# Optimization experiments

Measured on AMD Instinct MI355X. Metric: run time of the kernel, lower is better.

The kernel has to match this reference:

```python
import jax, jax.numpy as jnp
import numpy as np

NCONST = 100
NFEATS = 16
NCLASS = 5
NEFF = 6
NDYN = 6
BN_EPS = 1e-3  # keras BatchNormalization default epsilon


def _edge_indices(nconst):
    # itertools.product order, skipping self-pairs, matching _build_relation_matrices
    recv, send = [], []
    for i in range(nconst):
        for j in range(nconst):
            if i != j:
                recv.append(i)
                send.append(j)
    return np.asarray(recv, np.int32), np.asarray(send, np.int32)


def setup_inputs() -> dict:
    key = jax.random.key(0)
    ks = jax.random.split(key, 16)

    def w(k, shape, fan_in):
        return (jax.random.normal(k, shape, jnp.float32) / np.sqrt(fan_in)).astype(jnp.float32)

    inp = {
        "x": jax.random.normal(ks[0], (512, NCONST, NFEATS), jnp.float32),
        # batchnorm (inference-mode) params over the feature axis
        "bn_gamma": jnp.ones((NFEATS,), jnp.float32),
        "bn_beta": jnp.zeros((NFEATS,), jnp.float32),
        "bn_mean": jnp.zeros((NFEATS,), jnp.float32),
        "bn_var": jnp.ones((NFEATS,), jnp.float32),
        # fr: pointwise Conv1D == dense over last dim; 2*nfeats -> 30 -> 15 -> 6
        "fr_w1": w(ks[1], (2 * NFEATS, 30), 2 * NFEATS), "fr_b1": jnp.zeros((30,), jnp.float32),
        "fr_w2": w(ks[2], (30, 15), 30), "fr_b2": jnp.zeros((15,), jnp.float32),
        "fr_w3": w(ks[3], (15, NEFF), 15), "fr_b3": jnp.zeros((NEFF,), jnp.float32),
        # fo: (nfeats + neffects) -> 45 -> 22 -> 6
        "fo_w1": w(ks[4], (NFEATS + NEFF, 45), NFEATS + NEFF), "fo_b1": jnp.zeros((45,), jnp.float32),
        "fo_w2": w(ks[5], (45, 22), 45), "fo_b2": jnp.zeros((22,), jnp.float32),
        "fo_w3": w(ks[6], (22, NDYN), 22), "fo_b3": jnp.zeros((NDYN,), jnp.float32),
        # fc: ndyn -> 48 -> nclasses (softmax)
        "fc_w1": w(ks[7], (NDYN, 48), NDYN), "fc_b1": jnp.zeros((48,), jnp.float32),
        "fc_w2": w(ks[8], (48, NCLASS), 48), "fc_b2": jnp.zeros((NCLASS,), jnp.float32),
    }
    return inp


def reference(x, bn_gamma, bn_beta, bn_mean, bn_var,
              fr_w1, fr_b1, fr_w2, fr_b2, fr_w3, fr_b3,
              fo_w1, fo_b1, fo_w2, fo_b2, fo_w3, fo_b3,
              fc_w1, fc_b1, fc_w2, fc_b2):
    nconst = x.shape[1]
    recv_idx, send_idx = _edge_indices(nconst)  # static, shape (nedges,)

    # BatchNormalization (inference) over the feature axis: (B, N, F)
    xb = (x - bn_mean) * jax.lax.rsqrt(bn_var + BN_EPS) * bn_gamma + bn_beta

    # One-hot relation matmuls are exact gathers: (B, E, F) each.
    # Concat order matches Concatenate(axis=1)([receiver, sender]) pre-permute.
    fr_in = jnp.concatenate([xb[:, recv_idx, :], xb[:, send_idx, :]], axis=-1)  # (B, E, 2F)

    h = jax.nn.relu(fr_in @ fr_w1 + fr_b1)
    h = jax.nn.relu(h @ fr_w2 + fr_b2)
    effects = jax.nn.relu(h @ fr_w3 + fr_b3)  # (B, E, neff)

    # Multiplying by receiver_matrix^T is a scatter-add of edge effects to receiver nodes.
    agg = jnp.zeros((x.shape[0], nconst, effects.shape[-1]), effects.dtype)
    agg = agg.at[:, recv_idx, :].add(effects)  # (B, N, neff)

    fo_in = jnp.concatenate([xb, agg], axis=-1)  # (B, N, F + neff)
    d = jax.nn.relu(fo_in @ fo_w1 + fo_b1)
    d = jax.nn.relu(d @ fo_w2 + fo_b2)
    d = jax.nn.relu(d @ fo_w3 + fo_b3)  # (B, N, ndyn)

    fc_in = jnp.sum(d, axis=1)  # summation=True -> (B, ndyn)
    h = jax.nn.relu(fc_in @ fc_w1 + fc_b1)
    logits = h @ fc_w2 + fc_b2
    return jax.nn.softmax(logits, axis=-1)  # (B, nclasses)
```

## Files before the change

kernel.cpp:

```cpp
#include <hip/hip_runtime.h>
#include <math.h>

#define NCONST 100
#define NF     16
#define BLK    512

typedef _Float16 f16;
typedef _Float16 f16x8 __attribute__((ext_vector_type(8)));
typedef _Float16 f16x4 __attribute__((ext_vector_type(4)));
typedef float    f32x16 __attribute__((ext_vector_type(16)));

__global__ __launch_bounds__(BLK, 4) void convint_fused(
    const float* __restrict__ x,
    const float* __restrict__ bn_g, const float* __restrict__ bn_b,
    const float* __restrict__ bn_m, const float* __restrict__ bn_v,
    const float* __restrict__ frw1, const float* __restrict__ frb1,
    const float* __restrict__ frw2, const float* __restrict__ frb2,
    const float* __restrict__ frw3, const float* __restrict__ frb3,
    const float* __restrict__ fow1, const float* __restrict__ fob1,
    const float* __restrict__ fow2, const float* __restrict__ fob2,
    const float* __restrict__ fow3, const float* __restrict__ fob3,
    const float* __restrict__ fcw1, const float* __restrict__ fcb1,
    const float* __restrict__ fcw2, const float* __restrict__ fcb2,
    float* __restrict__ out)
{
    __shared__ float xbn[NCONST][NF];
    __shared__ float upool[7200];
    __shared__ float aggF[NCONST * 8];
    __shared__ float fcin[8];
    __shared__ float hfc[48];
    __shared__ float logits[8];

    char* const PrB = (char*)upool;
    char* const PsB = PrB + 8000;
    float (*const foh1)[48] = (float (*)[48])upool;
    float (*const foh2)[24] = (float (*)[24])(upool + 4800);

    const int b   = blockIdx.x;
    const int tid = threadIdx.x;
    const float* xb = x + (size_t)b * (NCONST * NF);

    for (int idx = tid; idx < NCONST * NF; idx += BLK) {
        int f = idx & 15;
        float sc = rsqrtf(bn_v[f] + 1e-3f) * bn_g[f];
        xbn[idx >> 4][f] = (xb[idx] - bn_m[f]) * sc + bn_b[f];
    }
    if (tid < 8) fcin[tid] = 0.f;
    __syncthreads();

    for (int idx = tid; idx < 1600; idx += BLK) {
        int n   = idx >> 4;
        int rem = idx & 15;
        int sel = rem >> 3;
        int oq  = rem & 7;
        int o0  = oq * 4;

        float xs[16];
        {
            const float4* xv = (const float4*)(&xbn[n][0]);
            float4 x0 = xv[0], x1 = xv[1], x2 = xv[2], x3 = xv[3];
            xs[0]=x0.x; xs[1]=x0.y; xs[2]=x0.z; xs[3]=x0.w;
            xs[4]=x1.x; xs[5]=x1.y; xs[6]=x1.z; xs[7]=x1.w;
            xs[8]=x2.x; xs[9]=x2.y; xs[10]=x2.z; xs[11]=x2.w;
            xs[12]=x3.x; xs[13]=x3.y; xs[14]=x3.z; xs[15]=x3.w;
        }
        float acc0 = (!sel) ? frb1[o0 + 0] : 0.f;
        float acc1 = (!sel) ? frb1[o0 + 1] : 0.f;
        float acc2 = (!sel && oq < 7) ? frb1[o0 + 2] : 0.f;
        float acc3 = (!sel && oq < 7) ? frb1[o0 + 3] : 0.f;
        const float* wbase = frw1 + sel * 16 * 30;
        const int wcol2 = (oq < 7) ? o0 + 2 : 28;
        #pragma unroll
        for (int f = 0; f < 16; ++f) {
            const float* wr = wbase + f * 30;
            float2 wa = *(const float2*)(wr + o0);
            float2 wb = *(const float2*)(wr + wcol2);
            acc0 = fmaf(xs[f], wa.x, acc0);
            acc1 = fmaf(xs[f], wa.y, acc1);
            acc2 = fmaf(xs[f], wb.x, acc2);
            acc3 = fmaf(xs[f], wb.y, acc3);
        }
        f16x4 hv;
        hv[0] = (f16)acc0;
        hv[1] = (f16)acc1;
        hv[2] = (oq < 7) ? (f16)acc2 : (sel ? (f16)0.f : (f16)1.f);
        hv[3] = (oq < 7) ? (f16)acc3 : (f16)0.f;
        int slot = oq >> 1;
        int sw = (slot & 2) | ((slot ^ (n >> 3)) & 1);
        *(f16x4*)((sel ? PsB : PrB) + n * 80 + sw * 16 + (oq & 1) * 8) = hv;
    }
    __syncthreads();

    {
        const int l  = tid & 63;
        const int wv = tid >> 6;
        const int e  = l & 31;
        const int hi = l >> 5;

        const int eC  = (e < 15) ? e : 14;
        const int eC3 = (e < 6)  ? e : 5;

        f16x8 bf1a, bf1b, bf2;
        #pragma unroll
        for (int m = 0; m < 8; ++m) {
            int ka  = hi * 8 + m;
            int kb_ = 16 + ka;
            float wa = frw2[ka * 15 + eC];
            float wb = (kb_ < 30) ? frw2[kb_ * 15 + eC] : frb2[eC];
            float w3 = (ka  < 15) ? frw3[ka * 6 + eC3]  : frb3[eC3];
            bf1a[m] = (e < 15)              ? (f16)wa : (f16)0.f;
            bf1b[m] = (e < 15 && kb_ < 31)  ? (f16)wb : (f16)0.f;
            bf2[m]  = (e < 6)               ? (f16)w3 : (f16)0.f;
        }
        f32x16 cz;
        #pragma unroll
        for (int r = 0; r < 16; ++r) cz[r] = 0.f;

        for (int i = wv; i < NCONST; i += 8) {
            const int pi = (i >> 3) & 1;
            const char* prp = PrB + i * 80 + ((hi ^ pi) * 16);
            f16x8 pra = *(const f16x8*)prp;
            f16x8 prb = *(const f16x8*)(prp + 32);
            float2 r2[2];
            r2[0].x = 0.f; r2[0].y = 0.f; r2[1].x = 0.f; r2[1].y = 0.f;

            int j = i + 1 + e; if (j >= 100) j -= 100;
            #pragma unroll
            for (int tb = 0; tb < 4; ++tb) {
                const int pj = (j >> 3) & 1;
                const char* psp = PsB + j * 80 + ((hi ^ pj) * 16);
                f16x8 psa = *(const f16x8*)psp;
                f16x8 psb = *(const f16x8*)(psp + 32);
                f16x8 h1a = pra + psa;
                f16x8 h1b = prb + psb;
                #pragma unroll
                for (int m = 0; m < 8; ++m) {
                    h1a[m] = (h1a[m] > (f16)0.f) ? h1a[m] : (f16)0.f;
                    h1b[m] = (h1b[m] > (f16)0.f) ? h1b[m] : (f16)0.f;
                }
                f32x16 c1 = __builtin_amdgcn_mfma_f32_32x32x16_f16(bf1a, h1a, cz, 0, 0, 0);
                c1 = __builtin_amdgcn_mfma_f32_32x32x16_f16(bf1b, h1b, c1, 0, 0, 0);

                float v7 = hi ? 1.0f : fmaxf(c1[7], 0.f);
                int pw0 = __builtin_bit_cast(int, __builtin_amdgcn_cvt_pkrtz(fmaxf(c1[0], 0.f), fmaxf(c1[1], 0.f)));
                int pw1 = __builtin_bit_cast(int, __builtin_amdgcn_cvt_pkrtz(fmaxf(c1[2], 0.f), fmaxf(c1[3], 0.f)));
                int pw2 = __builtin_bit_cast(int, __builtin_amdgcn_cvt_pkrtz(fmaxf(c1[4], 0.f), fmaxf(c1[5], 0.f)));
                int pw3 = __builtin_bit_cast(int, __builtin_amdgcn_cvt_pkrtz(fmaxf(c1[6], 0.f), v7));
                int s0 = hi ? pw0 : pw2;
                int s1 = hi ? pw1 : pw3;
                int r0 = __shfl_xor(s0, 32);
                int r1 = __shfl_xor(s1, 32);
                union { int w[4]; f16x8 v; } a2;
                a2.w[0] = hi ? r0  : pw0;
                a2.w[1] = hi ? r1  : pw1;
                a2.w[2] = hi ? pw2 : r0;
                a2.w[3] = hi ? pw3 : r1;

                f32x16 c2 = __builtin_amdgcn_mfma_f32_32x32x16_f16(a2.v, bf2, cz, 0, 0, 0);

                if (tb < 3) {
                    #pragma unroll
                    for (int p = 0; p < 8; ++p) {
                        r2[p & 1].x += fmaxf(c2[2 * p],     0.f);
                        r2[p & 1].y += fmaxf(c2[2 * p + 1], 0.f);
                    }
                } else if (hi == 0) {
                    r2[0].x += fmaxf(c2[0], 0.f);
                    r2[0].y += fmaxf(c2[1], 0.f);
                    r2[1].x += fmaxf(c2[2], 0.f);
                }
                j += 32; if (j >= 100) j -= 100;
            }
            float s = r2[0].x + r2[0].y + r2[1].x + r2[1].y;
            s += __shfl_xor(s, 32);
            if (hi == 0 && e < 6) aggF[i * 8 + e] = s;
        }
    }
    __syncthreads();

    for (int idx = tid; idx < NCONST * 45; idx += BLK) {
        int n = idx / 45, o = idx - n * 45;
        float acc = fob1[o];
        const float4* xv = (const float4*)(&xbn[n][0]);
        #pragma unroll
        for (int q = 0; q < 4; ++q) {
            float4 xq = xv[q];
            acc = fmaf(xq.x, fow1[(4 * q + 0) * 45 + o], acc);
            acc = fmaf(xq.y, fow1[(4 * q + 1) * 45 + o], acc);
            acc = fmaf(xq.z, fow1[(4 * q + 2) * 45 + o], acc);
            acc = fmaf(xq.w, fow1[(4 * q + 3) * 45 + o], acc);
        }
        const float4 a0 = *(const float4*)(&aggF[n * 8]);
        const float2 a1 = *(const float2*)(&aggF[n * 8 + 4]);
        acc = fmaf(a0.x, fow1[16 * 45 + o], acc);
        acc = fmaf(a0.y, fow1[17 * 45 + o], acc);
        acc = fmaf(a0.z, fow1[18 * 45 + o], acc);
        acc = fmaf(a0.w, fow1[19 * 45 + o], acc);
        acc = fmaf(a1.x, fow1[20 * 45 + o], acc);
        acc = fmaf(a1.y, fow1[21 * 45 + o], acc);
        foh1[n][o] = fmaxf(acc, 0.f);
    }
    __syncthreads();

    for (int idx = tid; idx < NCONST * 22; idx += BLK) {
        int n = idx / 22, o = idx - n * 22;
        float acc = fob2[o];
        const float4* hv = (const float4*)(&foh1[n][0]);
        #pragma unroll
        for (int q = 0; q < 11; ++q) {
            float4 h4 = hv[q];
            acc = fmaf(h4.x, fow2[(4 * q + 0) * 22 + o], acc);
            acc = fmaf(h4.y, fow2[(4 * q + 1) * 22 + o], acc);
            acc = fmaf(h4.z, fow2[(4 * q + 2) * 22 + o], acc);
            acc = fmaf(h4.w, fow2[(4 * q + 3) * 22 + o], acc);
        }
        acc = fmaf(foh1[n][44], fow2[44 * 22 + o], acc);
        foh2[n][o] = fmaxf(acc, 0.f);
    }
    __syncthreads();

    for (int idx = tid; idx < NCONST * 6; idx += BLK) {
        int n = idx / 6, c = idx - n * 6;
        float acc = fob3[c];
        const float4* hv = (const float4*)(&foh2[n][0]);
        #pragma unroll
        for (int q = 0; q < 5; ++q) {
            float4 h4 = hv[q];
            acc = fmaf(h4.x, fow3[(4 * q + 0) * 6 + c], acc);
            acc = fmaf(h4.y, fow3[(4 * q + 1) * 6 + c], acc);
            acc = fmaf(h4.z, fow3[(4 * q + 2) * 6 + c], acc);
            acc = fmaf(h4.w, fow3[(4 * q + 3) * 6 + c], acc);
        }
        acc = fmaf(foh2[n][20], fow3[20 * 6 + c], acc);
        acc = fmaf(foh2[n][21], fow3[21 * 6 + c], acc);
        atomicAdd(&fcin[c], fmaxf(acc, 0.f));
    }
    __syncthreads();

    if (tid < 48) {
        float acc = fcb1[tid];
        #pragma unroll
        for (int k = 0; k < 6; ++k) acc = fmaf(fcin[k], fcw1[k * 48 + tid], acc);
        hfc[tid] = fmaxf(acc, 0.f);
    }
    __syncthreads();
    if (tid < 5) {
        float acc = fcb2[tid];
        #pragma unroll
        for (int k = 0; k < 48; ++k) acc = fmaf(hfc[k], fcw2[k * 5 + tid], acc);
        logits[tid] = acc;
    }
    __syncthreads();
    if (tid == 0) {
        float m = logits[0];
        #pragma unroll
        for (int c = 1; c < 5; ++c) m = fmaxf(m, logits[c]);
        float ex[5], sum = 0.f;
        #pragma unroll
        for (int c = 0; c < 5; ++c) { ex[c] = __expf(logits[c] - m); sum += ex[c]; }
        float inv = 1.f / sum;
        #pragma unroll
        for (int c = 0; c < 5; ++c) out[(size_t)b * 5 + c] = ex[c] * inv;
    }
}

extern "C" void kernel_launch(void* const* d_in, const int* in_sizes, int n_in,
                              void* d_out, int out_size, void* d_ws, size_t ws_size,
                              hipStream_t stream) {
    const float* x     = (const float*)d_in[0];
    const float* bn_g  = (const float*)d_in[1];
    const float* bn_b  = (const float*)d_in[2];
    const float* bn_m  = (const float*)d_in[3];
    const float* bn_v  = (const float*)d_in[4];
    const float* frw1  = (const float*)d_in[5];
    const float* frb1  = (const float*)d_in[6];
    const float* frw2  = (const float*)d_in[7];
    const float* frb2  = (const float*)d_in[8];
    const float* frw3  = (const float*)d_in[9];
    const float* frb3  = (const float*)d_in[10];
    const float* fow1  = (const float*)d_in[11];
    const float* fob1  = (const float*)d_in[12];
    const float* fow2  = (const float*)d_in[13];
    const float* fob2  = (const float*)d_in[14];
    const float* fow3  = (const float*)d_in[15];
    const float* fob3  = (const float*)d_in[16];
    const float* fcw1  = (const float*)d_in[17];
    const float* fcb1  = (const float*)d_in[18];
    const float* fcw2  = (const float*)d_in[19];
    const float* fcb2  = (const float*)d_in[20];

    const int B = in_sizes[0] / (NCONST * NF);

    convint_fused<<<dim3(B), dim3(BLK), 0, stream>>>(
        x, bn_g, bn_b, bn_m, bn_v,
        frw1, frb1, frw2, frb2, frw3, frb3,
        fow1, fob1, fow2, fob2, fow3, fob3,
        fcw1, fcb1, fcw2, fcb2,
        (float*)d_out);
}
```

Baseline: 67.92 us.

## Split fused kernel into projection, edge, and output kernels via workspace

The single fused per-sample kernel becomes three kernels. The first computes the receiver/sender first-layer projections across two blocks per sample and writes them to a global workspace in fp16. The second runs the MFMA edge network with 1024-thread blocks (16 waves instead of 8) and writes the aggregated effects to global memory. The third recomputes batchnorm and runs the node and classifier MLPs. The aim is more parallelism and occupancy in each phase, at the cost of extra launches and global round-trips through the workspace.

```diff
diff --git a/kernel.cpp b/kernel.cpp
--- a/kernel.cpp
+++ b/kernel.cpp
@@ -3,20 +3,187 @@
 
 #define NCONST 100
 #define NF     16
-#define BLK    512
 
 typedef _Float16 f16;
 typedef _Float16 f16x8 __attribute__((ext_vector_type(8)));
 typedef _Float16 f16x4 __attribute__((ext_vector_type(4)));
 typedef float    f32x16 __attribute__((ext_vector_type(16)));
 
-__global__ __launch_bounds__(BLK, 4) void convint_fused(
+
+__global__ __launch_bounds__(512, 2) void k1_proj(
     const float* __restrict__ x,
     const float* __restrict__ bn_g, const float* __restrict__ bn_b,
     const float* __restrict__ bn_m, const float* __restrict__ bn_v,
     const float* __restrict__ frw1, const float* __restrict__ frb1,
+    f16* __restrict__ prps)
+{
+    __shared__ float xs[50][16];
+    const int b   = blockIdx.y;
+    const int n0  = blockIdx.x * 50;
+    const int tid = threadIdx.x;
+
+    for (int idx = tid; idx < 50 * 16; idx += 512) {
+        int f = idx & 15;
+        float sc = rsqrtf(bn_v[f] + 1e-3f) * bn_g[f];
+        xs[idx >> 4][f] = (x[((size_t)b * NCONST + n0) * NF + idx] - bn_m[f]) * sc + bn_b[f];
+    }
+    __syncthreads();
+
+    for (int idx = tid; idx < 800; idx += 512) {
+        int nL  = idx >> 4;
+        int rem = idx & 15;
+        int sel = rem >> 3;
+        int oq  = rem & 7;
+        int o0  = oq * 4;
+        int n   = n0 + nL;
+
+        float xv[16];
+        {
+            const float4* xp = (const float4*)(&xs[nL][0]);
+            float4 x0 = xp[0], x1 = xp[1], x2 = xp[2], x3 = xp[3];
+            xv[0]=x0.x; xv[1]=x0.y; xv[2]=x0.z; xv[3]=x0.w;
+            xv[4]=x1.x; xv[5]=x1.y; xv[6]=x1.z; xv[7]=x1.w;
+            xv[8]=x2.x; xv[9]=x2.y; xv[10]=x2.z; xv[11]=x2.w;
+            xv[12]=x3.x; xv[13]=x3.y; xv[14]=x3.z; xv[15]=x3.w;
+        }
+        float acc0 = (!sel) ? frb1[o0 + 0] : 0.f;
+        float acc1 = (!sel) ? frb1[o0 + 1] : 0.f;
+        float acc2 = (!sel && oq < 7) ? frb1[o0 + 2] : 0.f;
+        float acc3 = (!sel && oq < 7) ? frb1[o0 + 3] : 0.f;
+        const float* wbase = frw1 + sel * 16 * 30;
+        const int wcol2 = (oq < 7) ? o0 + 2 : 28;
+        #pragma unroll
+        for (int f = 0; f < 16; ++f) {
+            const float* wr = wbase + f * 30;
+            float2 wa = *(const float2*)(wr + o0);
+            float2 wb = *(const float2*)(wr + wcol2);
+            acc0 = fmaf(xv[f], wa.x, acc0);
+            acc1 = fmaf(xv[f], wa.y, acc1);
+            acc2 = fmaf(xv[f], wb.x, acc2);
+            acc3 = fmaf(xv[f], wb.y, acc3);
+        }
+        f16x4 hv;
+        hv[0] = (f16)acc0;
+        hv[1] = (f16)acc1;
+        hv[2] = (oq < 7) ? (f16)acc2 : (sel ? (f16)0.f : (f16)1.f);
+        hv[3] = (oq < 7) ? (f16)acc3 : (f16)0.f;
+        int slot = oq >> 1;
+        int sw = (slot & 2) | ((slot ^ (n >> 3)) & 1);
+        *(f16x4*)(prps + (size_t)b * 8192 + sel * 4000 + n * 40 + sw * 8 + (oq & 1) * 4) = hv;
+    }
+}
+
+__global__ __launch_bounds__(1024, 2) void k2_edge(
+    const f16* __restrict__ prps,
     const float* __restrict__ frw2, const float* __restrict__ frb2,
     const float* __restrict__ frw3, const float* __restrict__ frb3,
+    float* __restrict__ agg)
+{
+    __shared__ char P[16000];
+
+    const int b   = blockIdx.x;
+    const int tid = threadIdx.x;
+    {
+        const float4* src = (const float4*)(prps + (size_t)b * 8192);
+        float4* dst = (float4*)P;
+        if (tid < 1000) dst[tid] = src[tid];
+    }
+    __syncthreads();
+
+    const char* PrB = (const char*)P;
+    const char* PsB = (const char*)P + 8000;
+
+    const int l  = tid & 63;
+    const int wv = tid >> 6;
+    const int e  = l & 31;
+    const int hi = l >> 5;
+
+    const int eC  = (e < 15) ? e : 14;
+    const int eC3 = (e < 6)  ? e : 5;
+
+    f16x8 bf1a, bf1b, bf2;
+    #pragma unroll
+    for (int m = 0; m < 8; ++m) {
+        int ka  = hi * 8 + m;
+        int kb_ = 16 + ka;
+        float wa = frw2[ka * 15 + eC];
+        float wb = (kb_ < 30) ? frw2[kb_ * 15 + eC] : frb2[eC];
+        float w3 = (ka  < 15) ? frw3[ka * 6 + eC3]  : frb3[eC3];
+        bf1a[m] = (e < 15)              ? (f16)wa : (f16)0.f;
+        bf1b[m] = (e < 15 && kb_ < 31)  ? (f16)wb : (f16)0.f;
+        bf2[m]  = (e < 6)               ? (f16)w3 : (f16)0.f;
+    }
+    f32x16 cz;
+    #pragma unroll
+    for (int r = 0; r < 16; ++r) cz[r] = 0.f;
+
+    for (int i = wv; i < NCONST; i += 16) {
+        const int pi = (i >> 3) & 1;
+        const char* prp = PrB + i * 80 + ((hi ^ pi) * 16);
+        f16x8 pra = *(const f16x8*)prp;
+        f16x8 prb = *(const f16x8*)(prp + 32);
+        float2 r2[2];
+        r2[0].x = 0.f; r2[0].y = 0.f; r2[1].x = 0.f; r2[1].y = 0.f;
+
+        int j = i + 1 + e; if (j >= 100) j -= 100;
+        #pragma unroll
+        for (int tb = 0; tb < 4; ++tb) {
+            const int pj = (j >> 3) & 1;
+            const char* psp = PsB + j * 80 + ((hi ^ pj) * 16);
+            f16x8 psa = *(const f16x8*)psp;
+            f16x8 psb = *(const f16x8*)(psp + 32);
+            f16x8 h1a = pra + psa;
+            f16x8 h1b = prb + psb;
+            #pragma unroll
+            for (int m = 0; m < 8; ++m) {
+                h1a[m] = (h1a[m] > (f16)0.f) ? h1a[m] : (f16)0.f;
+                h1b[m] = (h1b[m] > (f16)0.f) ? h1b[m] : (f16)0.f;
+            }
+            f32x16 c1 = __builtin_amdgcn_mfma_f32_32x32x16_f16(bf1a, h1a, cz, 0, 0, 0);
+            c1 = __builtin_amdgcn_mfma_f32_32x32x16_f16(bf1b, h1b, c1, 0, 0, 0);
+
+            float v7 = hi ? 1.0f : fmaxf(c1[7], 0.f);
+            int pw0 = __builtin_bit_cast(int, __builtin_amdgcn_cvt_pkrtz(fmaxf(c1[0], 0.f), fmaxf(c1[1], 0.f)));
+            int pw1 = __builtin_bit_cast(int, __builtin_amdgcn_cvt_pkrtz(fmaxf(c1[2], 0.f), fmaxf(c1[3], 0.f)));
+            int pw2 = __builtin_bit_cast(int, __builtin_amdgcn_cvt_pkrtz(fmaxf(c1[4], 0.f), fmaxf(c1[5], 0.f)));
+            int pw3 = __builtin_bit_cast(int, __builtin_amdgcn_cvt_pkrtz(fmaxf(c1[6], 0.f), v7));
+            int s0 = hi ? pw0 : pw2;
+            int s1 = hi ? pw1 : pw3;
+            int r0 = __shfl_xor(s0, 32);
+            int r1 = __shfl_xor(s1, 32);
+            union { int w[4]; f16x8 v; } a2;
+            a2.w[0] = hi ? r0  : pw0;
+            a2.w[1] = hi ? r1  : pw1;
+            a2.w[2] = hi ? pw2 : r0;
+            a2.w[3] = hi ? pw3 : r1;
+
+            f32x16 c2 = __builtin_amdgcn_mfma_f32_32x32x16_f16(a2.v, bf2, cz, 0, 0, 0);
+
+            if (tb < 3) {
+                #pragma unroll
+                for (int p = 0; p < 8; ++p) {
+                    r2[p & 1].x += fmaxf(c2[2 * p],     0.f);
+                    r2[p & 1].y += fmaxf(c2[2 * p + 1], 0.f);
+                }
+            } else if (hi == 0) {
+                r2[0].x += fmaxf(c2[0], 0.f);
+                r2[0].y += fmaxf(c2[1], 0.f);
+                r2[1].x += fmaxf(c2[2], 0.f);
+            }
+            j += 32; if (j >= 100) j -= 100;
+        }
+        float s = r2[0].x + r2[0].y + r2[1].x + r2[1].y;
+        s += __shfl_xor(s, 32);
+        if (hi == 0 && e < 6)
+            agg[((size_t)b * NCONST + i) * 8 + e] = s;
+    }
+}
+
+__global__ __launch_bounds__(512, 2) void k3_out(
+    const float* __restrict__ x,
+    const float* __restrict__ bn_g, const float* __restrict__ bn_b,
+    const float* __restrict__ bn_m, const float* __restrict__ bn_v,
+    const float* __restrict__ agg_in,
     const float* __restrict__ fow1, const float* __restrict__ fob1,
     const float* __restrict__ fow2, const float* __restrict__ fob2,
     const float* __restrict__ fow3, const float* __restrict__ fob3,
@@ -24,164 +191,33 @@
     const float* __restrict__ fcw2, const float* __restrict__ fcb2,
     float* __restrict__ out)
 {
-    __shared__ float xbn[NCONST][NF];
-    __shared__ float upool[7200];
-    __shared__ float aggF[NCONST * 8];
+    __shared__ float xs[NCONST][16];
+    __shared__ float aggL[NCONST][8];
+    __shared__ float foh1[NCONST][48];
+    __shared__ float foh2[NCONST][24];
     __shared__ float fcin[8];
     __shared__ float hfc[48];
     __shared__ float logits[8];
 
-    char* const PrB = (char*)upool;
-    char* const PsB = PrB + 8000;
-    float (*const foh1)[48] = (float (*)[48])upool;
-    float (*const foh2)[24] = (float (*)[24])(upool + 4800);
-
     const int b   = blockIdx.x;
     const int tid = threadIdx.x;
-    const float* xb = x + (size_t)b * (NCONST * NF);
-
-    for (int idx = tid; idx < NCONST * NF; idx += BLK) {
+
+    for (int idx = tid; idx < NCONST * 16; idx += 512) {
         int f = idx & 15;
-        float sc = rsqrtf(bn_v[f] + 1e-3f) * bn_g[f];
-        xbn[idx >> 4][f] = (xb[idx] - bn_m[f]) * sc + bn_b[f];
+        float s = bn_g[f] * rsqrtf(bn_v[f] + 1e-3f);
+        xs[idx >> 4][f] = (x[(size_t)b * (NCONST * NF) + idx] - bn_m[f]) * s + bn_b[f];
+    }
+    for (int idx = tid; idx < NCONST * 6; idx += 512) {
+        int n = idx / 6, c = idx - n * 6;
+        aggL[n][c] = agg_in[((size_t)b * NCONST + n) * 8 + c];
     }
     if (tid < 8) fcin[tid] = 0.f;
     __syncthreads();
 
-    for (int idx = tid; idx < 1600; idx += BLK) {
-        int n   = idx >> 4;
-        int rem = idx & 15;
-        int sel = rem >> 3;
-        int oq  = rem & 7;
-        int o0  = oq * 4;
-
-        float xs[16];
-        {
-            const float4* xv = (const float4*)(&xbn[n][0]);
-            float4 x0 = xv[0], x1 = xv[1], x2 = xv[2], x3 = xv[3];
-            xs[0]=x0.x; xs[1]=x0.y; xs[2]=x0.z; xs[3]=x0.w;
-            xs[4]=x1.x; xs[5]=x1.y; xs[6]=x1.z; xs[7]=x1.w;
-            xs[8]=x2.x; xs[9]=x2.y; xs[10]=x2.z; xs[11]=x2.w;
-            xs[12]=x3.x; xs[13]=x3.y; xs[14]=x3.z; xs[15]=x3.w;
-        }
-        float acc0 = (!sel) ? frb1[o0 + 0] : 0.f;
-        float acc1 = (!sel) ? frb1[o0 + 1] : 0.f;
-        float acc2 = (!sel && oq < 7) ? frb1[o0 + 2] : 0.f;
-        float acc3 = (!sel && oq < 7) ? frb1[o0 + 3] : 0.f;
-        const float* wbase = frw1 + sel * 16 * 30;
-        const int wcol2 = (oq < 7) ? o0 + 2 : 28;
-        #pragma unroll
-        for (int f = 0; f < 16; ++f) {
-            const float* wr = wbase + f * 30;
-            float2 wa = *(const float2*)(wr + o0);
-            float2 wb = *(const float2*)(wr + wcol2);
-            acc0 = fmaf(xs[f], wa.x, acc0);
-            acc1 = fmaf(xs[f], wa.y, acc1);
-            acc2 = fmaf(xs[f], wb.x, acc2);
-            acc3 = fmaf(xs[f], wb.y, acc3);
-        }
-        f16x4 hv;
-        hv[0] = (f16)acc0;
-        hv[1] = (f16)acc1;
-        hv[2] = (oq < 7) ? (f16)acc2 : (sel ? (f16)0.f : (f16)1.f);
-        hv[3] = (oq < 7) ? (f16)acc3 : (f16)0.f;
-        int slot = oq >> 1;
-        int sw = (slot & 2) | ((slot ^ (n >> 3)) & 1);
-        *(f16x4*)((sel ? PsB : PrB) + n * 80 + sw * 16 + (oq & 1) * 8) = hv;
-    }
-    __syncthreads();
-
-    {
-        const int l  = tid & 63;
-        const int wv = tid >> 6;
-        const int e  = l & 31;
-        const int hi = l >> 5;
-
-        const int eC  = (e < 15) ? e : 14;
-        const int eC3 = (e < 6)  ? e : 5;
-
-        f16x8 bf1a, bf1b, bf2;
-        #pragma unroll
-        for (int m = 0; m < 8; ++m) {
-            int ka  = hi * 8 + m;
-            int kb_ = 16 + ka;
-            float wa = frw2[ka * 15 + eC];
-            float wb = (kb_ < 30) ? frw2[kb_ * 15 + eC] : frb2[eC];
-            float w3 = (ka  < 15) ? frw3[ka * 6 + eC3]  : frb3[eC3];
-            bf1a[m] = (e < 15)              ? (f16)wa : (f16)0.f;
-            bf1b[m] = (e < 15 && kb_ < 31)  ? (f16)wb : (f16)0.f;
-            bf2[m]  = (e < 6)               ? (f16)w3 : (f16)0.f;
-        }
-        f32x16 cz;
-        #pragma unroll
-        for (int r = 0; r < 16; ++r) cz[r] = 0.f;
-
-        for (int i = wv; i < NCONST; i += 8) {
-            const int pi = (i >> 3) & 1;
-            const char* prp = PrB + i * 80 + ((hi ^ pi) * 16);
-            f16x8 pra = *(const f16x8*)prp;
-            f16x8 prb = *(const f16x8*)(prp + 32);
-            float2 r2[2];
-            r2[0].x = 0.f; r2[0].y = 0.f; r2[1].x = 0.f; r2[1].y = 0.f;
-
-            int j = i + 1 + e; if (j >= 100) j -= 100;
-            #pragma unroll
-            for (int tb = 0; tb < 4; ++tb) {
-                const int pj = (j >> 3) & 1;
-                const char* psp = PsB + j * 80 + ((hi ^ pj) * 16);
-                f16x8 psa = *(const f16x8*)psp;
-                f16x8 psb = *(const f16x8*)(psp + 32);
-                f16x8 h1a = pra + psa;
-                f16x8 h1b = prb + psb;
-                #pragma unroll
-                for (int m = 0; m < 8; ++m) {
-                    h1a[m] = (h1a[m] > (f16)0.f) ? h1a[m] : (f16)0.f;
-                    h1b[m] = (h1b[m] > (f16)0.f) ? h1b[m] : (f16)0.f;
-                }
-                f32x16 c1 = __builtin_amdgcn_mfma_f32_32x32x16_f16(bf1a, h1a, cz, 0, 0, 0);
-                c1 = __builtin_amdgcn_mfma_f32_32x32x16_f16(bf1b, h1b, c1, 0, 0, 0);
-
-                float v7 = hi ? 1.0f : fmaxf(c1[7], 0.f);
-                int pw0 = __builtin_bit_cast(int, __builtin_amdgcn_cvt_pkrtz(fmaxf(c1[0], 0.f), fmaxf(c1[1], 0.f)));
-                int pw1 = __builtin_bit_cast(int, __builtin_amdgcn_cvt_pkrtz(fmaxf(c1[2], 0.f), fmaxf(c1[3], 0.f)));
-                int pw2 = __builtin_bit_cast(int, __builtin_amdgcn_cvt_pkrtz(fmaxf(c1[4], 0.f), fmaxf(c1[5], 0.f)));
-                int pw3 = __builtin_bit_cast(int, __builtin_amdgcn_cvt_pkrtz(fmaxf(c1[6], 0.f), v7));
-                int s0 = hi ? pw0 : pw2;
-                int s1 = hi ? pw1 : pw3;
-                int r0 = __shfl_xor(s0, 32);
-                int r1 = __shfl_xor(s1, 32);
-                union { int w[4]; f16x8 v; } a2;
-                a2.w[0] = hi ? r0  : pw0;
-                a2.w[1] = hi ? r1  : pw1;
-                a2.w[2] = hi ? pw2 : r0;
-                a2.w[3] = hi ? pw3 : r1;
-
-                f32x16 c2 = __builtin_amdgcn_mfma_f32_32x32x16_f16(a2.v, bf2, cz, 0, 0, 0);
-
-                if (tb < 3) {
-                    #pragma unroll
-                    for (int p = 0; p < 8; ++p) {
-                        r2[p & 1].x += fmaxf(c2[2 * p],     0.f);
-                        r2[p & 1].y += fmaxf(c2[2 * p + 1], 0.f);
-                    }
-                } else if (hi == 0) {
-                    r2[0].x += fmaxf(c2[0], 0.f);
-                    r2[0].y += fmaxf(c2[1], 0.f);
-                    r2[1].x += fmaxf(c2[2], 0.f);
-                }
-                j += 32; if (j >= 100) j -= 100;
-            }
-            float s = r2[0].x + r2[0].y + r2[1].x + r2[1].y;
-            s += __shfl_xor(s, 32);
-            if (hi == 0 && e < 6) aggF[i * 8 + e] = s;
-        }
-    }
-    __syncthreads();
-
-    for (int idx = tid; idx < NCONST * 45; idx += BLK) {
+    for (int idx = tid; idx < NCONST * 45; idx += 512) {
         int n = idx / 45, o = idx - n * 45;
         float acc = fob1[o];
-        const float4* xv = (const float4*)(&xbn[n][0]);
+        const float4* xv = (const float4*)(&xs[n][0]);
         #pragma unroll
         for (int q = 0; q < 4; ++q) {
             float4 xq = xv[q];
@@ -190,8 +226,8 @@
             acc = fmaf(xq.z, fow1[(4 * q + 2) * 45 + o], acc);
             acc = fmaf(xq.w, fow1[(4 * q + 3) * 45 + o], acc);
         }
-        const float4 a0 = *(const float4*)(&aggF[n * 8]);
-        const float2 a1 = *(const float2*)(&aggF[n * 8 + 4]);
+        const float4 a0 = *(const float4*)(&aggL[n][0]);
+        const float2 a1 = *(const float2*)(&aggL[n][4]);
         acc = fmaf(a0.x, fow1[16 * 45 + o], acc);
         acc = fmaf(a0.y, fow1[17 * 45 + o], acc);
         acc = fmaf(a0.z, fow1[18 * 45 + o], acc);
@@ -202,7 +238,7 @@
     }
     __syncthreads();
 
-    for (int idx = tid; idx < NCONST * 22; idx += BLK) {
+    for (int idx = tid; idx < NCONST * 22; idx += 512) {
         int n = idx / 22, o = idx - n * 22;
         float acc = fob2[o];
         const float4* hv = (const float4*)(&foh1[n][0]);
@@ -219,7 +255,7 @@
     }
     __syncthreads();
 
-    for (int idx = tid; idx < NCONST * 6; idx += BLK) {
+    for (int idx = tid; idx < NCONST * 6; idx += 512) {
         int n = idx / 6, c = idx - n * 6;
         float acc = fob3[c];
         const float4* hv = (const float4*)(&foh2[n][0]);
@@ -291,10 +327,15 @@
 
     const int B = in_sizes[0] / (NCONST * NF);
 
-    convint_fused<<<dim3(B), dim3(BLK), 0, stream>>>(
-        x, bn_g, bn_b, bn_m, bn_v,
-        frw1, frb1, frw2, frb2, frw3, frb3,
+    f16*   prps = (f16*)d_ws;
+    float* agg  = (float*)((char*)d_ws + (size_t)B * 16384);
+
+    k1_proj<<<dim3(2, B), dim3(512), 0, stream>>>(
+        x, bn_g, bn_b, bn_m, bn_v, frw1, frb1, prps);
+    k2_edge<<<dim3(B), dim3(1024), 0, stream>>>(
+        prps, frw2, frb2, frw3, frb3, agg);
+    k3_out<<<dim3(B), dim3(512), 0, stream>>>(
+        x, bn_g, bn_b, bn_m, bn_v, agg,
         fow1, fob1, fow2, fob2, fow3, fob3,
-        fcw1, fcb1, fcw2, fcb2,
-        (float*)d_out);
+        fcw1, fcb1, fcw2, fcb2, (float*)d_out);
 }
```

After: 91.43 us. 1.35x slower.

## Permute fr layer-2 output rows to avoid cross-half shuffle and transpose layer-3 MFMA

Applied to the files above, without the earlier changes.

Permutes the output columns of the second fr-layer weight matrix so the MFMA result lands in the register layout the third-layer MFMA expects as its B operand. This removes the per-edge-tile cross-half lane shuffles that previously rebuilt the A operand. The third-layer MFMA is swapped to put weights in A, so effects end up in the first four accumulator registers. Those are reduced over edges with a butterfly shuffle once per receiver instead of reducing 16 accumulators per tile. The tail-tile masking becomes a per-lane multiply by 0 or 1.

```diff
diff --git a/kernel.cpp b/kernel.cpp
--- a/kernel.cpp
+++ b/kernel.cpp
@@ -54,7 +54,6 @@
         int sel = rem >> 3;
         int oq  = rem & 7;
         int o0  = oq * 4;
-
         float xs[16];
         {
             const float4* xv = (const float4*)(&xbn[n][0]);
@@ -97,38 +96,46 @@
         const int e  = l & 31;
         const int hi = l >> 5;
 
-        const int eC  = (e < 15) ? e : 14;
-        const int eC3 = (e < 6)  ? e : 5;
-
-        f16x8 bf1a, bf1b, bf2;
+        const int o2p = (e >= 4 && e < 12) ? (e ^ 12) : e;
+        const bool o2v = (o2p < 15);
+        const int  o2c = o2v ? o2p : 0;
+        const bool o3v = (e < 6);
+        const int  o3c = o3v ? e : 0;
+
+        f16x8 bf1a, bf1b, bf2p;
         #pragma unroll
         for (int m = 0; m < 8; ++m) {
             int ka  = hi * 8 + m;
             int kb_ = 16 + ka;
-            float wa = frw2[ka * 15 + eC];
-            float wb = (kb_ < 30) ? frw2[kb_ * 15 + eC] : frb2[eC];
-            float w3 = (ka  < 15) ? frw3[ka * 6 + eC3]  : frb3[eC3];
-            bf1a[m] = (e < 15)              ? (f16)wa : (f16)0.f;
-            bf1b[m] = (e < 15 && kb_ < 31)  ? (f16)wb : (f16)0.f;
-            bf2[m]  = (e < 6)               ? (f16)w3 : (f16)0.f;
+            bf1a[m] = o2v ? (f16)frw2[ka * 15 + o2c] : (f16)0.f;
+            f16 wb = (f16)0.f;
+            if (o2v) {
+                if (kb_ < 30)       wb = (f16)frw2[kb_ * 15 + o2c];
+                else if (kb_ == 30) wb = (f16)frb2[o2c];
+            }
+            bf1b[m] = wb;
+            f16 w3 = (f16)0.f;
+            if (o3v) {
+                if (ka < 15)       w3 = (f16)frw3[ka * 6 + o3c];
+                else               w3 = (f16)frb3[o3c];
+            }
+            bf2p[m] = w3;
         }
         f32x16 cz;
         #pragma unroll
         for (int r = 0; r < 16; ++r) cz[r] = 0.f;
+        const float gtail = (e < 3) ? 1.f : 0.f;
 
         for (int i = wv; i < NCONST; i += 8) {
-            const int pi = (i >> 3) & 1;
-            const char* prp = PrB + i * 80 + ((hi ^ pi) * 16);
+            const char* prp = PrB + i * 80 + ((hi ^ ((i >> 3) & 1)) * 16);
             f16x8 pra = *(const f16x8*)prp;
             f16x8 prb = *(const f16x8*)(prp + 32);
-            float2 r2[2];
-            r2[0].x = 0.f; r2[0].y = 0.f; r2[1].x = 0.f; r2[1].y = 0.f;
+            float rc0 = 0.f, rc1 = 0.f, rc2 = 0.f, rc3 = 0.f;
 
             int j = i + 1 + e; if (j >= 100) j -= 100;
             #pragma unroll
             for (int tb = 0; tb < 4; ++tb) {
-                const int pj = (j >> 3) & 1;
-                const char* psp = PsB + j * 80 + ((hi ^ pj) * 16);
+                const char* psp = PsB + j * 80 + ((hi ^ ((j >> 3) & 1)) * 16);
                 f16x8 psa = *(const f16x8*)psp;
                 f16x8 psb = *(const f16x8*)(psp + 32);
                 f16x8 h1a = pra + psa;
@@ -141,39 +148,45 @@
                 f32x16 c1 = __builtin_amdgcn_mfma_f32_32x32x16_f16(bf1a, h1a, cz, 0, 0, 0);
                 c1 = __builtin_amdgcn_mfma_f32_32x32x16_f16(bf1b, h1b, c1, 0, 0, 0);
 
-                float v7 = hi ? 1.0f : fmaxf(c1[7], 0.f);
-                int pw0 = __builtin_bit_cast(int, __builtin_amdgcn_cvt_pkrtz(fmaxf(c1[0], 0.f), fmaxf(c1[1], 0.f)));
-                int pw1 = __builtin_bit_cast(int, __builtin_amdgcn_cvt_pkrtz(fmaxf(c1[2], 0.f), fmaxf(c1[3], 0.f)));
-                int pw2 = __builtin_bit_cast(int, __builtin_amdgcn_cvt_pkrtz(fmaxf(c1[4], 0.f), fmaxf(c1[5], 0.f)));
-                int pw3 = __builtin_bit_cast(int, __builtin_amdgcn_cvt_pkrtz(fmaxf(c1[6], 0.f), v7));
-                int s0 = hi ? pw0 : pw2;
-                int s1 = hi ? pw1 : pw3;
-                int r0 = __shfl_xor(s0, 32);
-                int r1 = __shfl_xor(s1, 32);
                 union { int w[4]; f16x8 v; } a2;
-                a2.w[0] = hi ? r0  : pw0;
-                a2.w[1] = hi ? r1  : pw1;
-                a2.w[2] = hi ? pw2 : r0;
-                a2.w[3] = hi ? pw3 : r1;
-
-                f32x16 c2 = __builtin_amdgcn_mfma_f32_32x32x16_f16(a2.v, bf2, cz, 0, 0, 0);
+                a2.w[0] = __builtin_bit_cast(int, __builtin_amdgcn_cvt_pkrtz(c1[0], c1[1]));
+                a2.w[1] = __builtin_bit_cast(int, __builtin_amdgcn_cvt_pkrtz(c1[2], c1[3]));
+                a2.w[2] = __builtin_bit_cast(int, __builtin_amdgcn_cvt_pkrtz(c1[4], c1[5]));
+                a2.w[3] = __builtin_bit_cast(int, __builtin_amdgcn_cvt_pkrtz(c1[6], c1[7]));
+                #pragma unroll
+                for (int m = 0; m < 8; ++m)
+                    a2.v[m] = (a2.v[m] > (f16)0.f) ? a2.v[m] : (f16)0.f;
+                a2.v[7] = hi ? (f16)1.f : a2.v[7];
+
+                f32x16 c2 = __builtin_amdgcn_mfma_f32_32x32x16_f16(bf2p, a2.v, cz, 0, 0, 0);
 
                 if (tb < 3) {
-                    #pragma unroll
-                    for (int p = 0; p < 8; ++p) {
-                        r2[p & 1].x += fmaxf(c2[2 * p],     0.f);
-                        r2[p & 1].y += fmaxf(c2[2 * p + 1], 0.f);
-                    }
-                } else if (hi == 0) {
-                    r2[0].x += fmaxf(c2[0], 0.f);
-                    r2[0].y += fmaxf(c2[1], 0.f);
-                    r2[1].x += fmaxf(c2[2], 0.f);
+                    rc0 += fmaxf(c2[0], 0.f);
+                    rc1 += fmaxf(c2[1], 0.f);
+                    rc2 += fmaxf(c2[2], 0.f);
+                    rc3 += fmaxf(c2[3], 0.f);
+                } else {
+                    rc0 = fmaf(gtail, fmaxf(c2[0], 0.f), rc0);
+                    rc1 = fmaf(gtail, fmaxf(c2[1], 0.f), rc1);
+                    rc2 = fmaf(gtail, fmaxf(c2[2], 0.f), rc2);
+                    rc3 = fmaf(gtail, fmaxf(c2[3], 0.f), rc3);
                 }
                 j += 32; if (j >= 100) j -= 100;
             }
-            float s = r2[0].x + r2[0].y + r2[1].x + r2[1].y;
-            s += __shfl_xor(s, 32);
-            if (hi == 0 && e < 6) aggF[i * 8 + e] = s;
+            #pragma unroll
+            for (int mk = 1; mk <= 16; mk <<= 1) {
+                rc0 += __shfl_xor(rc0, mk);
+                rc1 += __shfl_xor(rc1, mk);
+                rc2 += __shfl_xor(rc2, mk);
+                rc3 += __shfl_xor(rc3, mk);
+            }
+            if (l == 0) {
+                float4 v; v.x = rc0; v.y = rc1; v.z = rc2; v.w = rc3;
+                *(float4*)&aggF[i * 8] = v;
+            } else if (l == 32) {
+                float2 v; v.x = rc0; v.y = rc1;
+                *(float2*)&aggF[i * 8 + 4] = v;
+            }
         }
     }
     __syncthreads();
@@ -201,7 +214,6 @@
         foh1[n][o] = fmaxf(acc, 0.f);
     }
     __syncthreads();
-
     for (int idx = tid; idx < NCONST * 22; idx += BLK) {
         int n = idx / 22, o = idx - n * 22;
         float acc = fob2[o];
@@ -218,7 +230,6 @@
         foh2[n][o] = fmaxf(acc, 0.f);
     }
     __syncthreads();
-
     for (int idx = tid; idx < NCONST * 6; idx += BLK) {
         int n = idx / 6, c = idx - n * 6;
         float acc = fob3[c];
@@ -236,7 +247,6 @@
         atomicAdd(&fcin[c], fmaxf(acc, 0.f));
     }
     __syncthreads();
-
     if (tid < 48) {
         float acc = fcb1[tid];
         #pragma unroll
```

After: 61.96 us. -8.8%, faster.
